# Performance work log

Hardware: AMD Instinct MI355X
Metric: run time of the kernel (lower is better)

## Reference

```python
import jax, jax.numpy as jnp
import numpy as np
from functools import partial

N_MAX = 10
M = 10
T = 0.5
SQRT_T = T ** 0.5
HIDDEN = 2048
LATENT = 128
STROKE = 5
B = 128
INPUT_DIM = LATENT + STROKE  # 133
OUT_DIM = 6 * M + 3          # 63


def setup_inputs() -> dict:
    key = jax.random.key(0)
    ks = jax.random.split(key, 10)
    def init(k, shape, fan_in):
        return jax.random.normal(k, shape, dtype=jnp.float32) * (1.0 / np.sqrt(fan_in))
    return {
        "z": jax.random.normal(ks[0], (B, LATENT), dtype=jnp.float32),
        "N_s": jax.random.randint(ks[1], (B,), 0, N_MAX),
        "fc_in_w": init(ks[2], (2 * HIDDEN, LATENT), LATENT),
        "fc_in_b": jnp.zeros((2 * HIDDEN,), jnp.float32),
        "W_ih": init(ks[3], (4 * HIDDEN, INPUT_DIM), INPUT_DIM),
        "W_hh": init(ks[4], (4 * HIDDEN, HIDDEN), HIDDEN),
        "b_ih": jnp.zeros((4 * HIDDEN,), jnp.float32),
        "b_hh": jnp.zeros((4 * HIDDEN,), jnp.float32),
        "proj_w": init(ks[5], (OUT_DIM, HIDDEN), HIDDEN),
        "proj_b": jnp.zeros((OUT_DIM,), jnp.float32),
    }


def reference(z, N_s, fc_in_w, fc_in_b, W_ih, W_hh, b_ih, b_hh, proj_w, proj_b):
    # initial hidden/cell from latent: tanh(fc_in(z)) split into (h, c)
    hc = jnp.tanh(z @ fc_in_w.T + fc_in_b)          # (B, 2H)
    h0, c0 = hc[:, :HIDDEN], hc[:, HIDDEN:]
    keys = jax.random.split(jax.random.key(42), N_MAX)
    stroke0 = jnp.tile(jnp.array([0., 0., 1., 0., 0.], z.dtype), (B, 1))
    empty = jnp.array([0., 0., 0., 0., 1.], z.dtype)
    eye3 = jnp.eye(3, dtype=z.dtype)

    def step(carry, inp):
        h, c, stroke = carry
        i, key = inp
        # ---- LSTM cell (PyTorch gate order i,f,g,o) ----
        x = jnp.concatenate([z, stroke], axis=1)                     # (B, 133)
        gates = x @ W_ih.T + b_ih + h @ W_hh.T + b_hh                # (B, 4H)
        ig, fg, gg, og = jnp.split(gates, 4, axis=1)
        c_new = jax.nn.sigmoid(fg) * c + jax.nn.sigmoid(ig) * jnp.tanh(gg)
        h_new = jax.nn.sigmoid(og) * jnp.tanh(c_new)
        out = h_new @ proj_w.T + proj_b                              # (B, 63)
        # ---- MDN parameter extraction ----
        mix = out[:, :6 * M].reshape(B, M, 6)                        # (B, M, 6)
        pi = jax.nn.softmax(mix[:, :, 0] / T, axis=1)                # (B, M)
        mux, muy = mix[:, :, 1], mix[:, :, 2]
        sx = jnp.exp(mix[:, :, 3]) * SQRT_T
        sy = jnp.exp(mix[:, :, 4]) * SQRT_T
        rho = jnp.tanh(mix[:, :, 5])
        pen = jax.nn.softmax(out[:, 6 * M:] / T, axis=1)             # (B, 3)
        # ---- categorical sampling via cumsum + searchsorted ----
        k1, k2, k3, k4 = jax.random.split(key, 4)
        u = jax.random.uniform(k1, (B,), dtype=z.dtype)
        rx = jax.random.normal(k2, (B,), dtype=z.dtype)
        ry = jax.random.normal(k3, (B,), dtype=z.dtype)
        u2 = jax.random.uniform(k4, (B,), dtype=z.dtype)
        idx = jnp.clip(jnp.sum(jnp.cumsum(pi, axis=1) < u[:, None], axis=1), 0, M - 1)
        take = lambda a: jnp.take_along_axis(a, idx[:, None], axis=1)[:, 0]
        mx, my = take(mux), take(muy)
        sxg, syg, rg = take(sx), take(sy), take(rho)
        ox = mx + sxg * rx
        oy = my + syg * (rg * ox + jnp.sqrt(1.0 - rg ** 2) * ry)
        pidx = jnp.clip(jnp.sum(jnp.cumsum(pen, axis=1) < u2[:, None], axis=1), 0, 2)
        nxt = jnp.concatenate([ox[:, None], oy[:, None], eye3[pidx]], axis=1)  # (B, 5)
        # finished sequences emit the empty stroke
        nxt = jnp.where((i > N_s)[:, None], empty, nxt)
        return (h_new, c_new, nxt), nxt

    _, strokes = jax.lax.scan(step, (h0, c0, stroke0), (jnp.arange(N_MAX), keys))
    return strokes  # (N_max, B, stroke_dim)
```

## Files before the change

### kernel.cpp

```cpp
#include <hip/hip_runtime.h>
#include <stdint.h>
#include <stddef.h>

#define HID 2048
#define NB 128
#define NG 8192
#define ODIM 63

__device__ __forceinline__ void tf2x32(uint32_t k0, uint32_t k1,
                                       uint32_t x0, uint32_t x1,
                                       uint32_t& o0, uint32_t& o1) {
  uint32_t ks2 = k0 ^ k1 ^ 0x1BD11BDAu;
  x0 += k0; x1 += k1;
#define TF_ROTL(v,d) (((v)<<(d))|((v)>>(32-(d))))
#define TF_R(r) { x0 += x1; x1 = TF_ROTL(x1,r); x1 ^= x0; }
  TF_R(13) TF_R(15) TF_R(26) TF_R(6)
  x0 += k1;  x1 += ks2 + 1u;
  TF_R(17) TF_R(29) TF_R(16) TF_R(24)
  x0 += ks2; x1 += k0 + 2u;
  TF_R(13) TF_R(15) TF_R(26) TF_R(6)
  x0 += k0;  x1 += k1 + 3u;
  TF_R(17) TF_R(29) TF_R(16) TF_R(24)
  x0 += k1;  x1 += ks2 + 4u;
  TF_R(13) TF_R(15) TF_R(26) TF_R(6)
  x0 += ks2; x1 += k0 + 5u;
  o0 = x0; o1 = x1;
#undef TF_R
#undef TF_ROTL
}

__device__ __forceinline__ float unif01(uint32_t b) {
  return __uint_as_float((b >> 9) | 0x3f800000u) - 1.0f;
}

__device__ __forceinline__ float erfinv_xla(float x) {
  float t = x * x;
  float w = -log1pf(-t);
  float p;
  if (w < 5.0f) {
    w = w - 2.5f;
    p = 2.81022636e-08f;
    p = fmaf(p, w, 3.43273939e-07f);
    p = fmaf(p, w, -3.5233877e-06f);
    p = fmaf(p, w, -4.39150654e-06f);
    p = fmaf(p, w, 0.00021858087f);
    p = fmaf(p, w, -0.00125372503f);
    p = fmaf(p, w, -0.00417768164f);
    p = fmaf(p, w, 0.246640727f);
    p = fmaf(p, w, 1.50140941f);
  } else {
    w = sqrtf(w) - 3.0f;
    p = -0.000200214257f;
    p = fmaf(p, w, 0.000100950558f);
    p = fmaf(p, w, 0.00134934322f);
    p = fmaf(p, w, -0.00367342844f);
    p = fmaf(p, w, 0.00573950773f);
    p = fmaf(p, w, -0.0076224613f);
    p = fmaf(p, w, 0.00943887047f);
    p = fmaf(p, w, 1.00167406f);
    p = fmaf(p, w, 2.83297682f);
  }
  return p * x;
}

__device__ __forceinline__ float norm_from_bits(uint32_t b) {
  float f = unif01(b);
  float v = f * 2.0f + __uint_as_float(0xBF7FFFFFu);
  return __uint_as_float(0x3FB504F3u) * erfinv_xla(v);
}

__global__ void rand_kernel(float* __restrict__ u, float* __restrict__ rx,
                            float* __restrict__ ry, float* __restrict__ u2,
                            float* __restrict__ stroke) {
  const int i = blockIdx.x;
  const int l = threadIdx.x;
  if (i == 0) {
    stroke[l*5+0] = 0.f; stroke[l*5+1] = 0.f; stroke[l*5+2] = 1.f;
    stroke[l*5+3] = 0.f; stroke[l*5+4] = 0.f;
  }
  uint32_t ki0, ki1;
  tf2x32(0u, 42u, 0u, (uint32_t)i, ki0, ki1);
  uint32_t k1a,k1b,k2a,k2b,k3a,k3b,k4a,k4b;
  tf2x32(ki0, ki1, 0u, 0u, k1a, k1b);
  tf2x32(ki0, ki1, 0u, 1u, k2a, k2b);
  tf2x32(ki0, ki1, 0u, 2u, k3a, k3b);
  tf2x32(ki0, ki1, 0u, 3u, k4a, k4b);
  uint32_t o0, o1;
  const uint32_t ul = (uint32_t)l;
  tf2x32(k1a, k1b, 0u, ul, o0, o1);  u [i*NB + l] = unif01(o0 ^ o1);
  tf2x32(k2a, k2b, 0u, ul, o0, o1);  rx[i*NB + l] = norm_from_bits(o0 ^ o1);
  tf2x32(k3a, k3b, 0u, ul, o0, o1);  ry[i*NB + l] = norm_from_bits(o0 ^ o1);
  tf2x32(k4a, k4b, 0u, ul, o0, o1);  u2[i*NB + l] = unif01(o0 ^ o1);
}

#define BM 64
#define BN 64
#define BK 16
__global__ __launch_bounds__(256) void gemm_bt(
    const float* __restrict__ A, const float* __restrict__ B,
    int K, int ldb, int N, int mode,
    const float* __restrict__ bias1, const float* __restrict__ bias2,
    float* __restrict__ C, float* __restrict__ C2)
{
  __shared__ float As[BK][BM];
  __shared__ float Bs[BK][BN];
  const int tid = threadIdx.x;
  const int bm = blockIdx.y * BM;
  const int bn = blockIdx.x * BN;
  const int lr = tid >> 2;
  const int lk = (tid & 3) << 2;
  const int ty = tid >> 4, tx = tid & 15;
  const int mo = ty << 2, no = tx << 2;
  const bool b_aligned = ((ldb & 3) == 0);
  float acc[4][4] = {{0.f,0.f,0.f,0.f},{0.f,0.f,0.f,0.f},{0.f,0.f,0.f,0.f},{0.f,0.f,0.f,0.f}};

  for (int k0 = 0; k0 < K; k0 += BK) {
    const float* ap = A + (size_t)(bm + lr) * K + (k0 + lk);
    float4 av = *(const float4*)ap;
    As[lk+0][lr] = av.x; As[lk+1][lr] = av.y; As[lk+2][lr] = av.z; As[lk+3][lr] = av.w;
    const float* bp = B + (size_t)(bn + lr) * ldb + (k0 + lk);
    float4 bv;
    if (b_aligned) { bv = *(const float4*)bp; }
    else { bv.x = bp[0]; bv.y = bp[1]; bv.z = bp[2]; bv.w = bp[3]; }
    Bs[lk+0][lr] = bv.x; Bs[lk+1][lr] = bv.y; Bs[lk+2][lr] = bv.z; Bs[lk+3][lr] = bv.w;
    __syncthreads();
#pragma unroll
    for (int k = 0; k < BK; ++k) {
      float4 a = *(const float4*)&As[k][mo];
      float4 b = *(const float4*)&Bs[k][no];
      acc[0][0] = fmaf(a.x, b.x, acc[0][0]);
      acc[0][1] = fmaf(a.x, b.y, acc[0][1]);
      acc[0][2] = fmaf(a.x, b.z, acc[0][2]);
      acc[0][3] = fmaf(a.x, b.w, acc[0][3]);
      acc[1][0] = fmaf(a.y, b.x, acc[1][0]);
      acc[1][1] = fmaf(a.y, b.y, acc[1][1]);
      acc[1][2] = fmaf(a.y, b.z, acc[1][2]);
      acc[1][3] = fmaf(a.y, b.w, acc[1][3]);
      acc[2][0] = fmaf(a.z, b.x, acc[2][0]);
      acc[2][1] = fmaf(a.z, b.y, acc[2][1]);
      acc[2][2] = fmaf(a.z, b.z, acc[2][2]);
      acc[2][3] = fmaf(a.z, b.w, acc[2][3]);
      acc[3][0] = fmaf(a.w, b.x, acc[3][0]);
      acc[3][1] = fmaf(a.w, b.y, acc[3][1]);
      acc[3][2] = fmaf(a.w, b.z, acc[3][2]);
      acc[3][3] = fmaf(a.w, b.w, acc[3][3]);
    }
    __syncthreads();
  }

  const int n0 = bn + no;
#pragma unroll
  for (int i = 0; i < 4; ++i) {
    const int m = bm + mo + i;
    if (mode == 1) {
      float4 r;
      r.x = tanhf(acc[i][0] + bias1[n0+0]);
      r.y = tanhf(acc[i][1] + bias1[n0+1]);
      r.z = tanhf(acc[i][2] + bias1[n0+2]);
      r.w = tanhf(acc[i][3] + bias1[n0+3]);
      if (n0 < HID) *(float4*)&C [(size_t)m * HID + n0]        = r;
      else          *(float4*)&C2[(size_t)m * HID + (n0-HID)]  = r;
    } else {
      float4 r;
      r.x = acc[i][0] + bias1[n0+0] + bias2[n0+0];
      r.y = acc[i][1] + bias1[n0+1] + bias2[n0+1];
      r.z = acc[i][2] + bias1[n0+2] + bias2[n0+2];
      r.w = acc[i][3] + bias1[n0+3] + bias2[n0+3];
      *(float4*)&C[(size_t)m * N + n0] = r;
    }
  }
}

#define BK2 32
__global__ __launch_bounds__(256) void rec_gemm_lstm(
    const float* __restrict__ A,
    const float* __restrict__ W,
    const float* __restrict__ gz,
    const float* __restrict__ W_ih,
    const float* __restrict__ stroke,
    float* __restrict__ c,
    float* __restrict__ h_next)
{
  __shared__ float As[2][BK2][64];
  __shared__ float Bs[2][BK2][64];
  __shared__ float gt[64][68];
  const int tid = threadIdx.x;
  const int jc = blockIdx.x;
  const int bm = blockIdx.y * 64;
  const int j0 = jc * 16;

  const int sr = tid & 63;
  const int sk = (tid >> 6) << 3;
  const int brow = (sr >> 4) * HID + j0 + (sr & 15);
  const int mo = (tid >> 4) << 2;
  const int no = (tid & 15) << 2;

  float acc[4][4] = {{0.f,0.f,0.f,0.f},{0.f,0.f,0.f,0.f},{0.f,0.f,0.f,0.f},{0.f,0.f,0.f,0.f}};

  const float* abase = A + (size_t)(bm + sr) * HID + sk;
  const float* bbase = W + (size_t)brow * HID + sk;

#define STG(bi) do { \
    As[bi][sk+0][sr]=ra0.x; As[bi][sk+1][sr]=ra0.y; As[bi][sk+2][sr]=ra0.z; As[bi][sk+3][sr]=ra0.w; \
    As[bi][sk+4][sr]=ra1.x; As[bi][sk+5][sr]=ra1.y; As[bi][sk+6][sr]=ra1.z; As[bi][sk+7][sr]=ra1.w; \
    Bs[bi][sk+0][sr]=rb0.x; Bs[bi][sk+1][sr]=rb0.y; Bs[bi][sk+2][sr]=rb0.z; Bs[bi][sk+3][sr]=rb0.w; \
    Bs[bi][sk+4][sr]=rb1.x; Bs[bi][sk+5][sr]=rb1.y; Bs[bi][sk+6][sr]=rb1.z; Bs[bi][sk+7][sr]=rb1.w; \
  } while (0)

  float4 ra0 = *(const float4*)(abase);
  float4 ra1 = *(const float4*)(abase + 4);
  float4 rb0 = *(const float4*)(bbase);
  float4 rb1 = *(const float4*)(bbase + 4);
  STG(0);
  __syncthreads();

  int cur = 0;
  for (int t = 0; t < 64; ++t) {
    if (t < 63) {
      ra0 = *(const float4*)(abase + (t+1)*BK2);
      ra1 = *(const float4*)(abase + (t+1)*BK2 + 4);
      rb0 = *(const float4*)(bbase + (t+1)*BK2);
      rb1 = *(const float4*)(bbase + (t+1)*BK2 + 4);
    }
#pragma unroll
    for (int k = 0; k < BK2; ++k) {
      float4 a = *(const float4*)&As[cur][k][mo];
      float4 b = *(const float4*)&Bs[cur][k][no];
      acc[0][0] = fmaf(a.x, b.x, acc[0][0]);
      acc[0][1] = fmaf(a.x, b.y, acc[0][1]);
      acc[0][2] = fmaf(a.x, b.z, acc[0][2]);
      acc[0][3] = fmaf(a.x, b.w, acc[0][3]);
      acc[1][0] = fmaf(a.y, b.x, acc[1][0]);
      acc[1][1] = fmaf(a.y, b.y, acc[1][1]);
      acc[1][2] = fmaf(a.y, b.z, acc[1][2]);
      acc[1][3] = fmaf(a.y, b.w, acc[1][3]);
      acc[2][0] = fmaf(a.z, b.x, acc[2][0]);
      acc[2][1] = fmaf(a.z, b.y, acc[2][1]);
      acc[2][2] = fmaf(a.z, b.z, acc[2][2]);
      acc[2][3] = fmaf(a.z, b.w, acc[2][3]);
      acc[3][0] = fmaf(a.w, b.x, acc[3][0]);
      acc[3][1] = fmaf(a.w, b.y, acc[3][1]);
      acc[3][2] = fmaf(a.w, b.z, acc[3][2]);
      acc[3][3] = fmaf(a.w, b.w, acc[3][3]);
    }
    if (t < 63) STG(cur ^ 1);
    __syncthreads();
    cur ^= 1;
  }
#undef STG

  const int g = no >> 4;
#pragma unroll
  for (int i = 0; i < 4; ++i) {
    const int m = mo + i;
    float4 gzv = *(const float4*)&gz[(size_t)(bm + m) * NG + g * HID + j0 + (no & 15)];
    gt[m][no+0] = acc[i][0] + gzv.x;
    gt[m][no+1] = acc[i][1] + gzv.y;
    gt[m][no+2] = acc[i][2] + gzv.z;
    gt[m][no+3] = acc[i][3] + gzv.w;
  }
  __syncthreads();

#pragma unroll
  for (int p = 0; p < 4; ++p) {
    const int pid = p * 256 + tid;
    const int m  = pid >> 4;
    const int jj = pid & 15;
    const int gm = bm + m;
    const int col = j0 + jj;
    float gv[4];
    gv[0] = gt[m][jj];
    gv[1] = gt[m][16+jj];
    gv[2] = gt[m][32+jj];
    gv[3] = gt[m][48+jj];
    const float* st = stroke + gm*5;
    float s0 = st[0], s1 = st[1], s2 = st[2], s3 = st[3], s4 = st[4];
#pragma unroll
    for (int q = 0; q < 4; ++q) {
      const float* w = W_ih + (size_t)(q * HID + col) * 133 + 128;
      float t0 = gv[q];
      t0 = fmaf(s0, w[0], t0);
      t0 = fmaf(s1, w[1], t0);
      t0 = fmaf(s2, w[2], t0);
      t0 = fmaf(s3, w[3], t0);
      t0 = fmaf(s4, w[4], t0);
      gv[q] = t0;
    }
    float ig = 1.0f / (1.0f + expf(-gv[0]));
    float fg = 1.0f / (1.0f + expf(-gv[1]));
    float gg = tanhf(gv[2]);
    float og = 1.0f / (1.0f + expf(-gv[3]));
    const size_t idx = (size_t)gm * HID + col;
    float cn = fg * c[idx] + ig * gg;
    float hn = og * tanhf(cn);
    c[idx] = cn;
    h_next[idx] = hn;
  }
}

__global__ __launch_bounds__(256) void projsample(
    const float* __restrict__ h, const float* __restrict__ pw,
    const float* __restrict__ pb, const int* __restrict__ N_s,
    const float* __restrict__ u, const float* __restrict__ rx,
    const float* __restrict__ ry, const float* __restrict__ u2, int step,
    float* __restrict__ stroke, float* __restrict__ dout)
{
  __shared__ float hl[4*520];
  __shared__ float outs[64];
  const int b = blockIdx.x;
  const int t = threadIdx.x;
  const float* hp = h + (size_t)b * HID;
  {
    const int part = t >> 6;
    const int kk = (t * 8) & 511;
    float4 v0 = *(const float4*)&hp[t*8];
    float4 v1 = *(const float4*)&hp[t*8+4];
    *(float4*)&hl[part*520 + kk]     = v0;
    *(float4*)&hl[part*520 + kk + 4] = v1;
  }
  __syncthreads();
  if (t < 252) {
    const int n = t >> 2, part = t & 3;
    const float* wrow = pw + (size_t)n * HID + part * 512;
    const float* hh = hl + part * 520;
    float acc = 0.f;
#pragma unroll 4
    for (int k = 0; k < 512; k += 4) {
      float4 wv = *(const float4*)&wrow[k];
      float4 hv = *(const float4*)&hh[k];
      acc = fmaf(hv.x, wv.x, acc);
      acc = fmaf(hv.y, wv.y, acc);
      acc = fmaf(hv.z, wv.z, acc);
      acc = fmaf(hv.w, wv.w, acc);
    }
    acc += __shfl_xor(acc, 1);
    acc += __shfl_xor(acc, 2);
    if (part == 0) outs[n] = acc + pb[n];
  }
  __syncthreads();
  if (t == 0) {
    const float* o = outs;
    float xs[10];
    float mx = -3.402823466e+38f;
#pragma unroll
    for (int m = 0; m < 10; ++m) { xs[m] = o[6*m] * 2.0f; mx = fmaxf(mx, xs[m]); }
    float e[10]; float ssum = 0.f;
#pragma unroll
    for (int m = 0; m < 10; ++m) { e[m] = expf(xs[m] - mx); ssum += e[m]; }
    float uu = u[b];
    int cnt = 0; float csum = 0.f;
#pragma unroll
    for (int m = 0; m < 10; ++m) { csum += e[m] / ssum; cnt += (csum < uu) ? 1 : 0; }
    int idx = cnt > 9 ? 9 : cnt;
    float mux = o[6*idx+1], muy = o[6*idx+2];
    float sxg = expf(o[6*idx+3]) * __uint_as_float(0x3F3504F3u);
    float syg = expf(o[6*idx+4]) * __uint_as_float(0x3F3504F3u);
    float rg  = tanhf(o[6*idx+5]);
    float ox = mux + sxg * rx[b];
    float oy = muy + syg * (rg * ox + sqrtf(1.0f - rg*rg) * ry[b]);
    float p0 = o[60]*2.0f, p1 = o[61]*2.0f, p2 = o[62]*2.0f;
    float pmx = fmaxf(p0, fmaxf(p1, p2));
    float e0 = expf(p0-pmx), e1 = expf(p1-pmx), e2 = expf(p2-pmx);
    float es = e0+e1+e2;
    float uu2 = u2[b];
    int c2 = 0; float cs = 0.f;
    cs += e0/es; c2 += (cs < uu2) ? 1 : 0;
    cs += e1/es; c2 += (cs < uu2) ? 1 : 0;
    cs += e2/es; c2 += (cs < uu2) ? 1 : 0;
    int pidx = c2 > 2 ? 2 : c2;
    float nx0 = ox, nx1 = oy;
    float nx2 = (pidx==0)?1.f:0.f, nx3 = (pidx==1)?1.f:0.f, nx4 = (pidx==2)?1.f:0.f;
    if (step > N_s[b]) { nx0=0.f; nx1=0.f; nx2=0.f; nx3=0.f; nx4=1.f; }
    float* sp = stroke + b*5;
    sp[0]=nx0; sp[1]=nx1; sp[2]=nx2; sp[3]=nx3; sp[4]=nx4;
    float* dp = dout + b*5;
    dp[0]=nx0; dp[1]=nx1; dp[2]=nx2; dp[3]=nx3; dp[4]=nx4;
  }
}

extern "C" void kernel_launch(void* const* d_in, const int* in_sizes, int n_in,
                              void* d_out, int out_size, void* d_ws, size_t ws_size,
                              hipStream_t stream) {
  const float* z    = (const float*)d_in[0];
  const int*   N_s  = (const int*)  d_in[1];
  const float* fc_w = (const float*)d_in[2];
  const float* fc_b = (const float*)d_in[3];
  const float* W_ih = (const float*)d_in[4];
  const float* W_hh = (const float*)d_in[5];
  const float* b_ih = (const float*)d_in[6];
  const float* b_hh = (const float*)d_in[7];
  const float* pw   = (const float*)d_in[8];
  const float* pb   = (const float*)d_in[9];

  char* ws = (char*)d_ws;
  float* hA     = (float*)(ws + 0);
  float* c      = (float*)(ws + 1048576);
  float* gz     = (float*)(ws + 2097152);
  float* hB     = (float*)(ws + 6291456);
  float* u      = (float*)(ws + 10518528);
  float* rx     = (float*)(ws + 10523648);
  float* ry     = (float*)(ws + 10528768);
  float* u2     = (float*)(ws + 10533888);
  float* stroke = (float*)(ws + 10539008);
  float* dout   = (float*)d_out;

  rand_kernel<<<dim3(10), dim3(128), 0, stream>>>(u, rx, ry, u2, stroke);
  gemm_bt<<<dim3(4096/BN, NB/BM), dim3(256), 0, stream>>>(
      z, fc_w, 128, 128, 4096, 1, fc_b, nullptr, hA, c);
  gemm_bt<<<dim3(NG/BN, NB/BM), dim3(256), 0, stream>>>(
      z, W_ih, 128, 133, NG, 2, b_ih, b_hh, gz, nullptr);

  float* hbuf[2] = { hA, hB };
  for (int s = 0; s < 10; ++s) {
    float* hcur = hbuf[s & 1];
    float* hnxt = hbuf[(s + 1) & 1];
    rec_gemm_lstm<<<dim3(HID/16, NB/64), dim3(256), 0, stream>>>(
        hcur, W_hh, gz, W_ih, stroke, c, hnxt);
    projsample<<<dim3(NB), dim3(256), 0, stream>>>(
        hnxt, pw, pb, N_s, u + s*NB, rx + s*NB, ry + s*NB, u2 + s*NB, s,
        stroke, dout + s*NB*5);
  }
}
```

Measured before the change: 1.199 ms.

## Use split-bf16 MFMA for recurrent LSTM GEMM with hi/lo weight decomposition

Splits W_hh and the hidden state into high and low bf16 parts and computes the recurrent GEMM with three bf16 MFMA products per tile (hi*hi, hi*lo, lo*hi), which approximates fp32 accuracy using matrix cores instead of the scalar FMA tiled GEMM. The LSTM cell epilogue is fused and also emits the next step's hi/lo bf16 hidden state. It adds a per-call weight split pass over the 64MB W_hh and needs a larger workspace. When the workspace is too small it falls back to the old fp32 path. Operand loads go straight from global memory into MFMA registers without LDS staging.

After: 1.020 ms. 14.9% less time.

```diff
diff --git a/kernel.cpp b/kernel.cpp
--- a/kernel.cpp
+++ b/kernel.cpp
@@ -7,10 +7,22 @@
 #define NG 8192
 #define ODIM 63
 
-__device__ __forceinline__ void tf2x32(uint32_t k0, uint32_t k1,
-                                       uint32_t x0, uint32_t x1,
-                                       uint32_t& o0, uint32_t& o1) {
-  uint32_t ks2 = k0 ^ k1 ^ 0x1BD11BDAu;
+typedef unsigned int u32;
+typedef unsigned short u16;
+typedef short bf16x8 __attribute__((ext_vector_type(8)));
+typedef float f32x4 __attribute__((ext_vector_type(4)));
+
+__device__ __forceinline__ u16 f2bf(float x) {
+  u32 u = __float_as_uint(x);
+  return (u16)((u + 0x7FFFu + ((u >> 16) & 1u)) >> 16);
+}
+__device__ __forceinline__ float bf2f(u16 b) {
+  return __uint_as_float(((u32)b) << 16);
+}
+
+__device__ __forceinline__ void tf2x32(u32 k0, u32 k1, u32 x0, u32 x1,
+                                       u32& o0, u32& o1) {
+  u32 ks2 = k0 ^ k1 ^ 0x1BD11BDAu;
   x0 += k0; x1 += k1;
 #define TF_ROTL(v,d) (((v)<<(d))|((v)>>(32-(d))))
 #define TF_R(r) { x0 += x1; x1 = TF_ROTL(x1,r); x1 ^= x0; }
@@ -29,7 +41,7 @@
 #undef TF_ROTL
 }
 
-__device__ __forceinline__ float unif01(uint32_t b) {
+__device__ __forceinline__ float unif01(u32 b) {
   return __uint_as_float((b >> 9) | 0x3f800000u) - 1.0f;
 }
 
@@ -63,7 +75,7 @@
   return p * x;
 }
 
-__device__ __forceinline__ float norm_from_bits(uint32_t b) {
+__device__ __forceinline__ float norm_from_bits(u32 b) {
   float f = unif01(b);
   float v = f * 2.0f + __uint_as_float(0xBF7FFFFFu);
   return __uint_as_float(0x3FB504F3u) * erfinv_xla(v);
@@ -78,19 +90,38 @@
     stroke[l*5+0] = 0.f; stroke[l*5+1] = 0.f; stroke[l*5+2] = 1.f;
     stroke[l*5+3] = 0.f; stroke[l*5+4] = 0.f;
   }
-  uint32_t ki0, ki1;
-  tf2x32(0u, 42u, 0u, (uint32_t)i, ki0, ki1);
-  uint32_t k1a,k1b,k2a,k2b,k3a,k3b,k4a,k4b;
+  u32 ki0, ki1;
+  tf2x32(0u, 42u, 0u, (u32)i, ki0, ki1);
+  u32 k1a,k1b,k2a,k2b,k3a,k3b,k4a,k4b;
   tf2x32(ki0, ki1, 0u, 0u, k1a, k1b);
   tf2x32(ki0, ki1, 0u, 1u, k2a, k2b);
   tf2x32(ki0, ki1, 0u, 2u, k3a, k3b);
   tf2x32(ki0, ki1, 0u, 3u, k4a, k4b);
-  uint32_t o0, o1;
-  const uint32_t ul = (uint32_t)l;
+  u32 o0, o1;
+  const u32 ul = (u32)l;
   tf2x32(k1a, k1b, 0u, ul, o0, o1);  u [i*NB + l] = unif01(o0 ^ o1);
   tf2x32(k2a, k2b, 0u, ul, o0, o1);  rx[i*NB + l] = norm_from_bits(o0 ^ o1);
   tf2x32(k3a, k3b, 0u, ul, o0, o1);  ry[i*NB + l] = norm_from_bits(o0 ^ o1);
   tf2x32(k4a, k4b, 0u, ul, o0, o1);  u2[i*NB + l] = unif01(o0 ^ o1);
+}
+
+__global__ __launch_bounds__(256) void w_split(const float* __restrict__ W,
+                                               u16* __restrict__ Whi,
+                                               u16* __restrict__ Wlo) {
+  const int i8 = (blockIdx.x * 256 + threadIdx.x) * 8;
+  float4 v0 = *(const float4*)&W[i8];
+  float4 v1 = *(const float4*)&W[i8 + 4];
+  float v[8] = {v0.x, v0.y, v0.z, v0.w, v1.x, v1.y, v1.z, v1.w};
+  u32 hp[4], lp[4];
+#pragma unroll
+  for (int j = 0; j < 4; ++j) {
+    u16 h0 = f2bf(v[2*j]),   l0 = f2bf(v[2*j]   - bf2f(h0));
+    u16 h1 = f2bf(v[2*j+1]), l1 = f2bf(v[2*j+1] - bf2f(h1));
+    hp[j] = (u32)h0 | ((u32)h1 << 16);
+    lp[j] = (u32)l0 | ((u32)l1 << 16);
+  }
+  *(uint4*)&Whi[i8] = make_uint4(hp[0], hp[1], hp[2], hp[3]);
+  *(uint4*)&Wlo[i8] = make_uint4(lp[0], lp[1], lp[2], lp[3]);
 }
 
 #define BM 64
@@ -100,7 +131,8 @@
     const float* __restrict__ A, const float* __restrict__ B,
     int K, int ldb, int N, int mode,
     const float* __restrict__ bias1, const float* __restrict__ bias2,
-    float* __restrict__ C, float* __restrict__ C2)
+    float* __restrict__ C, float* __restrict__ C2,
+    u16* __restrict__ Chi, u16* __restrict__ Clo)
 {
   __shared__ float As[BK][BM];
   __shared__ float Bs[BK][BN];
@@ -158,8 +190,24 @@
       r.y = tanhf(acc[i][1] + bias1[n0+1]);
       r.z = tanhf(acc[i][2] + bias1[n0+2]);
       r.w = tanhf(acc[i][3] + bias1[n0+3]);
-      if (n0 < HID) *(float4*)&C [(size_t)m * HID + n0]        = r;
-      else          *(float4*)&C2[(size_t)m * HID + (n0-HID)]  = r;
+      if (n0 < HID) {
+        *(float4*)&C[(size_t)m * HID + n0] = r;
+        if (Chi) {
+          float rv[4] = {r.x, r.y, r.z, r.w};
+          u32 hp[2], lp[2];
+#pragma unroll
+          for (int j = 0; j < 2; ++j) {
+            u16 h0 = f2bf(rv[2*j]),   l0 = f2bf(rv[2*j]   - bf2f(h0));
+            u16 h1 = f2bf(rv[2*j+1]), l1 = f2bf(rv[2*j+1] - bf2f(h1));
+            hp[j] = (u32)h0 | ((u32)h1 << 16);
+            lp[j] = (u32)l0 | ((u32)l1 << 16);
+          }
+          *(uint2*)&Chi[(size_t)m * HID + n0] = make_uint2(hp[0], hp[1]);
+          *(uint2*)&Clo[(size_t)m * HID + n0] = make_uint2(lp[0], lp[1]);
+        }
+      } else {
+        *(float4*)&C2[(size_t)m * HID + (n0-HID)] = r;
+      }
     } else {
       float4 r;
       r.x = acc[i][0] + bias1[n0+0] + bias2[n0+0];
@@ -171,14 +219,136 @@
   }
 }
 
-#define BK2 32
-__global__ __launch_bounds__(256) void rec_gemm_lstm(
-    const float* __restrict__ A,
-    const float* __restrict__ W,
+__global__ __launch_bounds__(256) void rec_mfma_lstm(
+    const u16* __restrict__ hHi, const u16* __restrict__ hLo,
+    const u16* __restrict__ WHi, const u16* __restrict__ WLo,
     const float* __restrict__ gz,
     const float* __restrict__ W_ih,
     const float* __restrict__ stroke,
     float* __restrict__ c,
+    float* __restrict__ h_next,
+    u16* __restrict__ hHiN, u16* __restrict__ hLoN)
+{
+  __shared__ float gt[4][32][33];
+  const int tid = threadIdx.x;
+  const int jc = blockIdx.x;
+  const int mb = blockIdx.y;
+  const int g  = tid >> 6;
+  const int l  = tid & 63;
+  const int lr = l & 15;
+  const int lk = (l >> 4) * 8;
+
+  f32x4 acc00 = {0.f,0.f,0.f,0.f}, acc01 = {0.f,0.f,0.f,0.f};
+  f32x4 acc10 = {0.f,0.f,0.f,0.f}, acc11 = {0.f,0.f,0.f,0.f};
+
+  const u16* pa0h = hHi + (size_t)(mb*32 +      lr) * HID + lk;
+  const u16* pa1h = hHi + (size_t)(mb*32 + 16 + lr) * HID + lk;
+  const u16* pa0l = hLo + (size_t)(mb*32 +      lr) * HID + lk;
+  const u16* pa1l = hLo + (size_t)(mb*32 + 16 + lr) * HID + lk;
+  const size_t bn0 = (size_t)(g*HID + jc*32 +      lr) * HID + lk;
+  const size_t bn1 = (size_t)(g*HID + jc*32 + 16 + lr) * HID + lk;
+  const u16* pb0h = WHi + bn0;
+  const u16* pb1h = WHi + bn1;
+  const u16* pb0l = WLo + bn0;
+  const u16* pb1l = WLo + bn1;
+
+#pragma unroll 2
+  for (int k0 = 0; k0 < HID; k0 += 32) {
+    bf16x8 a0h = *(const bf16x8*)(pa0h + k0);
+    bf16x8 a1h = *(const bf16x8*)(pa1h + k0);
+    bf16x8 a0l = *(const bf16x8*)(pa0l + k0);
+    bf16x8 a1l = *(const bf16x8*)(pa1l + k0);
+    bf16x8 b0h = *(const bf16x8*)(pb0h + k0);
+    bf16x8 b1h = *(const bf16x8*)(pb1h + k0);
+    bf16x8 b0l = *(const bf16x8*)(pb0l + k0);
+    bf16x8 b1l = *(const bf16x8*)(pb1l + k0);
+    acc00 = __builtin_amdgcn_mfma_f32_16x16x32_bf16(a0h, b0h, acc00, 0, 0, 0);
+    acc00 = __builtin_amdgcn_mfma_f32_16x16x32_bf16(a0h, b0l, acc00, 0, 0, 0);
+    acc00 = __builtin_amdgcn_mfma_f32_16x16x32_bf16(a0l, b0h, acc00, 0, 0, 0);
+    acc01 = __builtin_amdgcn_mfma_f32_16x16x32_bf16(a0h, b1h, acc01, 0, 0, 0);
+    acc01 = __builtin_amdgcn_mfma_f32_16x16x32_bf16(a0h, b1l, acc01, 0, 0, 0);
+    acc01 = __builtin_amdgcn_mfma_f32_16x16x32_bf16(a0l, b1h, acc01, 0, 0, 0);
+    acc10 = __builtin_amdgcn_mfma_f32_16x16x32_bf16(a1h, b0h, acc10, 0, 0, 0);
+    acc10 = __builtin_amdgcn_mfma_f32_16x16x32_bf16(a1h, b0l, acc10, 0, 0, 0);
+    acc10 = __builtin_amdgcn_mfma_f32_16x16x32_bf16(a1l, b0h, acc10, 0, 0, 0);
+    acc11 = __builtin_amdgcn_mfma_f32_16x16x32_bf16(a1h, b1h, acc11, 0, 0, 0);
+    acc11 = __builtin_amdgcn_mfma_f32_16x16x32_bf16(a1h, b1l, acc11, 0, 0, 0);
+    acc11 = __builtin_amdgcn_mfma_f32_16x16x32_bf16(a1l, b1h, acc11, 0, 0, 0);
+  }
+
+  {
+    const int rr = (l >> 4) * 4;
+#pragma unroll
+    for (int r = 0; r < 4; ++r) {
+      gt[g][ 0 + rr + r][ 0 + lr] = acc00[r];
+      gt[g][ 0 + rr + r][16 + lr] = acc01[r];
+      gt[g][16 + rr + r][ 0 + lr] = acc10[r];
+      gt[g][16 + rr + r][16 + lr] = acc11[r];
+    }
+  }
+  __syncthreads();
+
+  const int m  = tid >> 3;
+  const int j4 = (tid & 7) * 4;
+  const int gm = mb*32 + m;
+  const int col = jc*32 + j4;
+  float gv[4][4];
+#pragma unroll
+  for (int q = 0; q < 4; ++q) {
+    float4 z4 = *(const float4*)&gz[(size_t)gm * NG + q * HID + col];
+    gv[q][0] = z4.x + gt[q][m][j4+0];
+    gv[q][1] = z4.y + gt[q][m][j4+1];
+    gv[q][2] = z4.z + gt[q][m][j4+2];
+    gv[q][3] = z4.w + gt[q][m][j4+3];
+  }
+  const float* st = stroke + gm*5;
+  float s0 = st[0], s1 = st[1], s2 = st[2], s3 = st[3], s4 = st[4];
+#pragma unroll
+  for (int q = 0; q < 4; ++q) {
+#pragma unroll
+    for (int i = 0; i < 4; ++i) {
+      const float* w = W_ih + (size_t)(q * HID + col + i) * 133 + 128;
+      float t0 = gv[q][i];
+      t0 = fmaf(s0, w[0], t0);
+      t0 = fmaf(s1, w[1], t0);
+      t0 = fmaf(s2, w[2], t0);
+      t0 = fmaf(s3, w[3], t0);
+      t0 = fmaf(s4, w[4], t0);
+      gv[q][i] = t0;
+    }
+  }
+  const size_t cidx = (size_t)gm * HID + col;
+  float4 cv = *(float4*)&c[cidx];
+  float cin[4] = {cv.x, cv.y, cv.z, cv.w};
+  float hn[4], cn[4];
+#pragma unroll
+  for (int i = 0; i < 4; ++i) {
+    float ig = 1.0f / (1.0f + expf(-gv[0][i]));
+    float fg = 1.0f / (1.0f + expf(-gv[1][i]));
+    float gg = tanhf(gv[2][i]);
+    float og = 1.0f / (1.0f + expf(-gv[3][i]));
+    cn[i] = fg * cin[i] + ig * gg;
+    hn[i] = og * tanhf(cn[i]);
+  }
+  *(float4*)&c[cidx]      = make_float4(cn[0], cn[1], cn[2], cn[3]);
+  *(float4*)&h_next[cidx] = make_float4(hn[0], hn[1], hn[2], hn[3]);
+  u32 hp[2], lp[2];
+#pragma unroll
+  for (int j = 0; j < 2; ++j) {
+    u16 h0 = f2bf(hn[2*j]),   l0 = f2bf(hn[2*j]   - bf2f(h0));
+    u16 h1 = f2bf(hn[2*j+1]), l1 = f2bf(hn[2*j+1] - bf2f(h1));
+    hp[j] = (u32)h0 | ((u32)h1 << 16);
+    lp[j] = (u32)l0 | ((u32)l1 << 16);
+  }
+  *(uint2*)&hHiN[cidx] = make_uint2(hp[0], hp[1]);
+  *(uint2*)&hLoN[cidx] = make_uint2(lp[0], lp[1]);
+}
+
+#define BK2 32
+__global__ __launch_bounds__(256) void rec_gemm_lstm(
+    const float* __restrict__ A, const float* __restrict__ W,
+    const float* __restrict__ gz, const float* __restrict__ W_ih,
+    const float* __restrict__ stroke, float* __restrict__ c,
     float* __restrict__ h_next)
 {
   __shared__ float As[2][BK2][64];
@@ -188,32 +358,26 @@
   const int jc = blockIdx.x;
   const int bm = blockIdx.y * 64;
   const int j0 = jc * 16;
-
   const int sr = tid & 63;
   const int sk = (tid >> 6) << 3;
   const int brow = (sr >> 4) * HID + j0 + (sr & 15);
   const int mo = (tid >> 4) << 2;
   const int no = (tid & 15) << 2;
-
   float acc[4][4] = {{0.f,0.f,0.f,0.f},{0.f,0.f,0.f,0.f},{0.f,0.f,0.f,0.f},{0.f,0.f,0.f,0.f}};
-
   const float* abase = A + (size_t)(bm + sr) * HID + sk;
   const float* bbase = W + (size_t)brow * HID + sk;
-
 #define STG(bi) do { \
     As[bi][sk+0][sr]=ra0.x; As[bi][sk+1][sr]=ra0.y; As[bi][sk+2][sr]=ra0.z; As[bi][sk+3][sr]=ra0.w; \
     As[bi][sk+4][sr]=ra1.x; As[bi][sk+5][sr]=ra1.y; As[bi][sk+6][sr]=ra1.z; As[bi][sk+7][sr]=ra1.w; \
     Bs[bi][sk+0][sr]=rb0.x; Bs[bi][sk+1][sr]=rb0.y; Bs[bi][sk+2][sr]=rb0.z; Bs[bi][sk+3][sr]=rb0.w; \
     Bs[bi][sk+4][sr]=rb1.x; Bs[bi][sk+5][sr]=rb1.y; Bs[bi][sk+6][sr]=rb1.z; Bs[bi][sk+7][sr]=rb1.w; \
   } while (0)
-
   float4 ra0 = *(const float4*)(abase);
   float4 ra1 = *(const float4*)(abase + 4);
   float4 rb0 = *(const float4*)(bbase);
   float4 rb1 = *(const float4*)(bbase + 4);
   STG(0);
   __syncthreads();
-
   int cur = 0;
   for (int t = 0; t < 64; ++t) {
     if (t < 63) {
@@ -248,7 +412,6 @@
     cur ^= 1;
   }
 #undef STG
-
   const int g = no >> 4;
 #pragma unroll
   for (int i = 0; i < 4; ++i) {
@@ -260,7 +423,6 @@
     gt[m][no+3] = acc[i][3] + gzv.w;
   }
   __syncthreads();
-
 #pragma unroll
   for (int p = 0; p < 4; ++p) {
     const int pid = p * 256 + tid;
@@ -292,9 +454,9 @@
     float og = 1.0f / (1.0f + expf(-gv[3]));
     const size_t idx = (size_t)gm * HID + col;
     float cn = fg * c[idx] + ig * gg;
-    float hn = og * tanhf(cn);
+    float hnv = og * tanhf(cn);
     c[idx] = cn;
-    h_next[idx] = hn;
+    h_next[idx] = hnv;
   }
 }
 
@@ -402,22 +564,44 @@
   float* ry     = (float*)(ws + 10528768);
   float* u2     = (float*)(ws + 10533888);
   float* stroke = (float*)(ws + 10539008);
+  u16*   Whi    = (u16*)(ws + 11534336);
+  u16*   Wlo    = (u16*)(ws + 45088768);
+  u16*   hHiA   = (u16*)(ws + 78643200);
+  u16*   hLoA   = (u16*)(ws + 79167488);
+  u16*   hHiB   = (u16*)(ws + 79691776);
+  u16*   hLoB   = (u16*)(ws + 80216064);
   float* dout   = (float*)d_out;
+
+  const bool fast = (ws_size >= 80740352ull);
 
   rand_kernel<<<dim3(10), dim3(128), 0, stream>>>(u, rx, ry, u2, stroke);
   gemm_bt<<<dim3(4096/BN, NB/BM), dim3(256), 0, stream>>>(
-      z, fc_w, 128, 128, 4096, 1, fc_b, nullptr, hA, c);
+      z, fc_w, 128, 128, 4096, 1, fc_b, nullptr, hA, c,
+      fast ? hHiA : nullptr, fast ? hLoA : nullptr);
   gemm_bt<<<dim3(NG/BN, NB/BM), dim3(256), 0, stream>>>(
-      z, W_ih, 128, 133, NG, 2, b_ih, b_hh, gz, nullptr);
-
-  float* hbuf[2] = { hA, hB };
-  for (int s = 0; s < 10; ++s) {
-    float* hcur = hbuf[s & 1];
-    float* hnxt = hbuf[(s + 1) & 1];
-    rec_gemm_lstm<<<dim3(HID/16, NB/64), dim3(256), 0, stream>>>(
-        hcur, W_hh, gz, W_ih, stroke, c, hnxt);
-    projsample<<<dim3(NB), dim3(256), 0, stream>>>(
-        hnxt, pw, pb, N_s, u + s*NB, rx + s*NB, ry + s*NB, u2 + s*NB, s,
-        stroke, dout + s*NB*5);
-  }
-}
+      z, W_ih, 128, 133, NG, 2, b_ih, b_hh, gz, nullptr, nullptr, nullptr);
+
+  if (fast) {
+    w_split<<<dim3(8192), dim3(256), 0, stream>>>(W_hh, Whi, Wlo);
+    u16* hhi[2] = { hHiA, hHiB };
+    u16* hlo[2] = { hLoA, hLoB };
+    float* hbuf[2] = { hA, hB };
+    for (int s = 0; s < 10; ++s) {
+      rec_mfma_lstm<<<dim3(64, 4), dim3(256), 0, stream>>>(
+          hhi[s & 1], hlo[s & 1], Whi, Wlo, gz, W_ih, stroke, c,
+          hbuf[(s + 1) & 1], hhi[(s + 1) & 1], hlo[(s + 1) & 1]);
+      projsample<<<dim3(NB), dim3(256), 0, stream>>>(
+          hbuf[(s + 1) & 1], pw, pb, N_s, u + s*NB, rx + s*NB, ry + s*NB,
+          u2 + s*NB, s, stroke, dout + s*NB*5);
+    }
+  } else {
+    float* hbuf[2] = { hA, hB };
+    for (int s = 0; s < 10; ++s) {
+      rec_gemm_lstm<<<dim3(HID/16, NB/64), dim3(256), 0, stream>>>(
+          hbuf[s & 1], W_hh, gz, W_ih, stroke, c, hbuf[(s + 1) & 1]);
+      projsample<<<dim3(NB), dim3(256), 0, stream>>>(
+          hbuf[(s + 1) & 1], pw, pb, N_s, u + s*NB, rx + s*NB, ry + s*NB,
+          u2 + s*NB, s, stroke, dout + s*NB*5);
+    }
+  }
+}
```
